# Kernel tuning notes

Hardware: AMD Instinct MI355X
Metric: run time of the kernel (lower is better)

## Reference

```python
import jax, jax.numpy as jnp
import numpy as np

K = 11          # kernel_size
SIGMA = 1.5
CH = 3          # image channels


def _gaussian_kernel(ch):
    coords = jnp.arange(K, dtype=jnp.float32) - (K - 1) / 2
    g = jnp.exp(-coords ** 2 / (2 * SIGMA ** 2))
    g = g / g.sum()
    k2d = jnp.outer(g, g)                       # [K, K]
    return jnp.tile(k2d[None, None], (ch, 1, 1, 1))  # [C, 1, K, K] depthwise


def setup_inputs() -> dict:
    key = jax.random.key(0)
    kx, ky = jax.random.split(key)
    x = jax.random.normal(kx, (32, CH, 512, 512), dtype=jnp.float32)
    y = jax.random.normal(ky, (32, CH, 512, 512), dtype=jnp.float32)
    kernel = _gaussian_kernel(CH)
    return {"x": x, "y": y, "kernel": kernel}


def _blur(v, kernel):
    # depthwise 2D Gaussian blur, SAME padding (K odd)
    c = v.shape[1]
    pad = K // 2
    return jax.lax.conv_general_dilated(
        v, kernel, window_strides=(1, 1), padding=[(pad, pad), (pad, pad)],
        dimension_numbers=("NCHW", "OIHW", "NCHW"), feature_group_count=c)


def reference(x, y, kernel):
    C1 = 0.01 ** 2
    C2 = 0.03 ** 2
    mu_x = _blur(x, kernel)
    mu_y = _blur(y, kernel)
    sigma_x = _blur(x * x, kernel) - mu_x ** 2
    sigma_y = _blur(y * y, kernel) - mu_y ** 2
    sigma_xy = _blur(x * y, kernel) - mu_x * mu_y
    ssim_num = (2 * mu_x * mu_y + C1) * (2 * sigma_xy + C2)
    ssim_den = (mu_x ** 2 + mu_y ** 2 + C1) * (sigma_x + sigma_y + C2)
    ssim = ssim_num / (ssim_den + 1e-8)
    return ((1.0 - ssim) / 2.0).mean()
```

## Files before the change

kernel.cpp:

```cpp
#include <hip/hip_runtime.h>
#include <hip/hip_bf16.h>

#define IMG    512
#define KSZ    11
#define HALO   5
#define STRIP  64
#define PANEL  16
#define NSTEP  (IMG/PANEL)
#define RRING  48
#define RPAIR  24
#define FCOLS  74
#define FSTR   88

typedef short bf16x8 __attribute__((ext_vector_type(8)));
typedef float f32x4  __attribute__((ext_vector_type(4)));

union S8 { bf16x8 v; ushort u16[8]; uint u32[4]; };

__device__ __forceinline__ ushort f2bf(float f) {
    union { __hip_bfloat16 h; ushort u; } c;
    c.h = __float2bfloat16(f);
    return c.u;
}


__global__ __launch_bounds__(256)
void dssim_mfma_kernel(const float* __restrict__ x,
                       const float* __restrict__ y,
                       const float* __restrict__ kern,
                       float* __restrict__ out)
{
    __shared__ float  sgf[16];
    __shared__ ushort gext[64];
    __shared__ ushort Fbuf[5][PANEL][FSTR];
    __shared__ ushort Ring[RPAIR][5][68][2];
    __shared__ float  wsum[4];

    const int tid = threadIdx.x;
    const int l   = tid & 63;
    const int wv  = tid >> 6;
    const int q   = l >> 4;
    const int cj  = l & 15;
    const int wcb = wv * 16 + cj;

    if (tid < KSZ) {
        float s = 0.f;
        #pragma unroll
        for (int j = 0; j < KSZ; ++j) s += kern[tid * KSZ + j];
        sgf[tid] = s;
    }
    for (int i = tid; i < 5 * PANEL * FSTR / 2; i += 256) ((uint*)Fbuf)[i] = 0u;
    for (int i = tid; i < 3 * 5 * 68; i += 256) ((uint*)Ring)[i] = 0u;
    __syncthreads();

    if (tid < 64) {
        const int d = tid - 16;
        gext[tid] = (d >= 0 && d < KSZ) ? f2bf(sgf[d]) : (ushort)0;
    }
    __syncthreads();

    S8 tg;
    #pragma unroll
    for (int ii = 0; ii < 8; ++ii)
        tg.u16[ii] = gext[16 + q * 8 + ii - cj];

    const int plane  = blockIdx.z;
    const int cstrip = blockIdx.x * STRIP;
    const int base   = plane * (IMG * IMG);

    const int srow = tid >> 4;
    const int scol = tid & 15;
    int  gcols[5]; bool coks[5];
    #pragma unroll
    for (int m = 0; m < 5; ++m) {
        const int cl = scol + 16 * m;
        gcols[m] = cstrip - HALO + cl;
        coks[m]  = (cl < FCOLS) && (gcols[m] >= 0) && (gcols[m] < IMG);
    }
    float2 pf[5];

    const ushort* aptr = &Fbuf[0][cj][wv * 16 + q * 8];

    const float C1 = 1e-4f, C2 = 9e-4f;
    const f32x4 z = {0.f, 0.f, 0.f, 0.f};
    float local = 0.f;

    {
        const int r  = srow;
        const int rb = base + r * IMG;
        #pragma unroll
        for (int m = 0; m < 5; ++m) {
            float xv = 0.f, yv = 0.f;
            if (coks[m]) { xv = x[rb + gcols[m]]; yv = y[rb + gcols[m]]; }
            pf[m] = make_float2(xv, yv);
        }
        #pragma unroll
        for (int m = 0; m < 5; ++m) {
            const int cl = scol + 16 * m;
            if (cl < FCOLS) {
                const float fx = pf[m].x, fy = pf[m].y;
                Fbuf[0][srow][cl] = f2bf(fx);
                Fbuf[1][srow][cl] = f2bf(fy);
                Fbuf[2][srow][cl] = f2bf(fx * fx);
                Fbuf[3][srow][cl] = f2bf(fy * fy);
                Fbuf[4][srow][cl] = f2bf(fx * fy);
            }
        }
    }
    __syncthreads();

    for (int t = 0; t <= NSTEP; ++t) {
        {
            const int pb = 16 * (t % 3) + HALO;
            #pragma unroll
            for (int f = 0; f < 5; ++f) {
                S8 a;
                a.v = *(const bf16x8*)(aptr + f * (PANEL * FSTR));
                f32x4 d = __builtin_amdgcn_mfma_f32_16x16x32_bf16(a.v, tg.v, z, 0, 0, 0);
                #pragma unroll
                for (int r = 0; r < 4; ++r) {
                    int rr = pb + q * 4 + r;
                    if (rr >= RRING) rr -= RRING;
                    Ring[rr >> 1][f][wcb][rr & 1] = f2bf(d[r]);
                }
            }
        }

        if (t < NSTEP) {
            const int r   = (t + 1) * PANEL + srow;
            const bool rok = (r < IMG);
            const int rb  = base + r * IMG;
            #pragma unroll
            for (int m = 0; m < 5; ++m) {
                float xv = 0.f, yv = 0.f;
                if (rok && coks[m]) { xv = x[rb + gcols[m]]; yv = y[rb + gcols[m]]; }
                pf[m] = make_float2(xv, yv);
            }
        }

        __syncthreads();

        if (t >= 1) {
            const int s   = t - 1;
            const int pbs = (8 * s) % RPAIR;
            int pr[4];
            #pragma unroll
            for (int ii = 0; ii < 4; ++ii) {
                int v = pbs + q * 4 + ii;
                if (v >= RPAIR) v -= RPAIR;
                pr[ii] = v;
            }
            f32x4 vf[5];
            #pragma unroll
            for (int f = 0; f < 5; ++f) {
                S8 b;
                #pragma unroll
                for (int ii = 0; ii < 4; ++ii)
                    b.u32[ii] = *(const uint*)&Ring[pr[ii]][f][wcb][0];
                vf[f] = __builtin_amdgcn_mfma_f32_16x16x32_bf16(tg.v, b.v, z, 0, 0, 0);
            }
            #pragma unroll
            for (int r = 0; r < 4; ++r) {
                const float mx  = vf[0][r], my  = vf[1][r];
                const float exx = vf[2][r], eyy = vf[3][r], exy = vf[4][r];
                const float sxv = fmaf(-mx, mx, exx);
                const float syv = fmaf(-my, my, eyy);
                const float sxy = fmaf(-mx, my, exy);
                const float num = fmaf(2.f, mx * my, C1) * fmaf(2.f, sxy, C2);
                const float den = fmaf(mx, mx, fmaf(my, my, C1)) * (sxv + syv + C2);
                const float ssim = __fdividef(num, den + 1e-8f);
                local += (1.f - ssim) * 0.5f;
            }
        }

        if (t < NSTEP) {
            #pragma unroll
            for (int m = 0; m < 5; ++m) {
                const int cl = scol + 16 * m;
                if (cl < FCOLS) {
                    const float fx = pf[m].x, fy = pf[m].y;
                    Fbuf[0][srow][cl] = f2bf(fx);
                    Fbuf[1][srow][cl] = f2bf(fy);
                    Fbuf[2][srow][cl] = f2bf(fx * fx);
                    Fbuf[3][srow][cl] = f2bf(fy * fy);
                    Fbuf[4][srow][cl] = f2bf(fx * fy);
                }
            }
        }
        __syncthreads();
    }

    #pragma unroll
    for (int o = 32; o > 0; o >>= 1) local += __shfl_down(local, o, 64);
    if (l == 0) wsum[wv] = local;
    __syncthreads();
    if (tid == 0) {
        const float s = wsum[0] + wsum[1] + wsum[2] + wsum[3];
        atomicAdd(out, s * (1.f / 25165824.f));
    }
}

extern "C" void kernel_launch(void* const* d_in, const int* in_sizes, int n_in,
                              void* d_out, int out_size, void* d_ws, size_t ws_size,
                              hipStream_t stream)
{
    const float* x    = (const float*)d_in[0];
    const float* y    = (const float*)d_in[1];
    const float* kern = (const float*)d_in[2];
    float* out = (float*)d_out;

    hipMemsetAsync(out, 0, sizeof(float), stream);

    dim3 grid(IMG / STRIP, 1, 32 * 3);
    dssim_mfma_kernel<<<grid, 256, 0, stream>>>(x, y, kern, out);
}
```

Measured before the change: 92.42 us.

## Pack bf16 pairs into 32-bit LDS words for staging and ring buffers

Restructures the shared-memory staging so each thread loads column pairs and writes packed bf16x2 words using v_cvt_pk_bf16_f32 and v_pk_mul_f32, instead of scalar 16-bit stores. The ring buffer becomes a flat 32-bit array, with the horizontal MFMA output stored as two packed words and the vertical tap vector shifted by one to match the new row alignment. The aim is fewer LDS store instructions and conversion ops per panel. It risks index or alignment mistakes in the remapped ring offsets and new bank-conflict patterns.

```diff
diff --git a/kernel.cpp b/kernel.cpp
--- a/kernel.cpp
+++ b/kernel.cpp
@@ -6,17 +6,26 @@
 #define HALO   5
 #define STRIP  64
 #define PANEL  16
-#define NSTEP  (IMG/PANEL)
-#define RRING  48
-#define RPAIR  24
-#define FCOLS  74
-#define FSTR   88
+#define NSTEP  32
+#define PAIRS  37
+#define FSTR32 44
+#define FROW   704
+#define RSTR32 340
 
 typedef short bf16x8 __attribute__((ext_vector_type(8)));
 typedef float f32x4  __attribute__((ext_vector_type(4)));
-
 union S8 { bf16x8 v; ushort u16[8]; uint u32[4]; };
 
+__device__ __forceinline__ uint cvtpk(float lo, float hi) {
+    uint r;
+    asm("v_cvt_pk_bf16_f32 %0, %1, %2" : "=v"(r) : "v"(lo), "v"(hi));
+    return r;
+}
+__device__ __forceinline__ float2 pk_mul(float2 a, float2 b) {
+    float2 d;
+    asm("v_pk_mul_f32 %0, %1, %2" : "=v"(d) : "v"(a), "v"(b));
+    return d;
+}
 __device__ __forceinline__ ushort f2bf(float f) {
     union { __hip_bfloat16 h; ushort u; } c;
     c.h = __float2bfloat16(f);
@@ -32,8 +41,8 @@
 {
     __shared__ float  sgf[16];
     __shared__ ushort gext[64];
-    __shared__ ushort Fbuf[5][PANEL][FSTR];
-    __shared__ ushort Ring[RPAIR][5][68][2];
+    __shared__ uint   Fbuf32[5 * FROW];
+    __shared__ uint   Ring32[24 * RSTR32];
     __shared__ float  wsum[4];
 
     const int tid = threadIdx.x;
@@ -49,115 +58,116 @@
         for (int j = 0; j < KSZ; ++j) s += kern[tid * KSZ + j];
         sgf[tid] = s;
     }
-    for (int i = tid; i < 5 * PANEL * FSTR / 2; i += 256) ((uint*)Fbuf)[i] = 0u;
-    for (int i = tid; i < 3 * 5 * 68; i += 256) ((uint*)Ring)[i] = 0u;
-    __syncthreads();
-
+    for (int i = tid; i < 5 * FROW; i += 256) Fbuf32[i] = 0u;
+    for (int i = tid; i < 3 * RSTR32; i += 256) Ring32[i] = 0u;
+    __syncthreads();
     if (tid < 64) {
         const int d = tid - 16;
         gext[tid] = (d >= 0 && d < KSZ) ? f2bf(sgf[d]) : (ushort)0;
     }
     __syncthreads();
 
-    S8 tg;
+    S8 tgh, tgv;
     #pragma unroll
-    for (int ii = 0; ii < 8; ++ii)
-        tg.u16[ii] = gext[16 + q * 8 + ii - cj];
+    for (int ii = 0; ii < 8; ++ii) {
+        tgh.u16[ii] = gext[16 + q * 8 + ii - cj];
+        tgv.u16[ii] = gext[15 + q * 8 + ii - cj];
+    }
 
     const int plane  = blockIdx.z;
     const int cstrip = blockIdx.x * STRIP;
     const int base   = plane * (IMG * IMG);
 
     const int srow = tid >> 4;
-    const int scol = tid & 15;
-    int  gcols[5]; bool coks[5];
+    const int sp   = tid & 15;
+    int gcol0[3], gcol1[3], wo[3];
+    bool ok0[3], ok1[3];
     #pragma unroll
-    for (int m = 0; m < 5; ++m) {
-        const int cl = scol + 16 * m;
-        gcols[m] = cstrip - HALO + cl;
-        coks[m]  = (cl < FCOLS) && (gcols[m] >= 0) && (gcols[m] < IMG);
-    }
-    float2 pf[5];
-
-    const ushort* aptr = &Fbuf[0][cj][wv * 16 + q * 8];
-
+    for (int m = 0; m < 3; ++m) {
+        const int p  = sp + 16 * m;
+        const bool pa = (p < PAIRS);
+        const int c0 = cstrip - HALO + 2 * p;
+        gcol0[m] = c0;  gcol1[m] = c0 + 1;
+        ok0[m] = pa && (c0 >= 0) && (c0 < IMG);
+        ok1[m] = pa && (c0 + 1 >= 0) && (c0 + 1 < IMG);
+        wo[m]  = srow * FSTR32 + p;
+    }
+    float2 px[3], py[3];
+
+    auto prefetch = [&](int pn) {
+        const int r    = pn * PANEL + srow;
+        const bool rok = (r < IMG);
+        const int rb   = base + r * IMG;
+        #pragma unroll
+        for (int m = 0; m < 3; ++m) {
+            float a0 = 0.f, a1 = 0.f, b0 = 0.f, b1 = 0.f;
+            if (rok && ok0[m]) { a0 = x[rb + gcol0[m]]; b0 = y[rb + gcol0[m]]; }
+            if (rok && ok1[m]) { a1 = x[rb + gcol1[m]]; b1 = y[rb + gcol1[m]]; }
+            px[m] = make_float2(a0, a1);
+            py[m] = make_float2(b0, b1);
+        }
+    };
+    auto commit = [&]() {
+        #pragma unroll
+        for (int m = 0; m < 3; ++m) {
+            if (m < 2 || sp < PAIRS - 32) {
+                const float2 vx = px[m], vy = py[m];
+                const float2 xx = pk_mul(vx, vx);
+                const float2 yy = pk_mul(vy, vy);
+                const float2 xy = pk_mul(vx, vy);
+                Fbuf32[0 * FROW + wo[m]] = cvtpk(vx.x, vx.y);
+                Fbuf32[1 * FROW + wo[m]] = cvtpk(vy.x, vy.y);
+                Fbuf32[2 * FROW + wo[m]] = cvtpk(xx.x, xx.y);
+                Fbuf32[3 * FROW + wo[m]] = cvtpk(yy.x, yy.y);
+                Fbuf32[4 * FROW + wo[m]] = cvtpk(xy.x, xy.y);
+            }
+        }
+    };
+
+    prefetch(0);
+    commit();
+    __syncthreads();
+
+    const f32x4 z0 = {0.f, 0.f, 0.f, 0.f};
     const float C1 = 1e-4f, C2 = 9e-4f;
-    const f32x4 z = {0.f, 0.f, 0.f, 0.f};
+    const int aoff = cj * FSTR32 + wv * 8 + q * 4;
     float local = 0.f;
-
-    {
-        const int r  = srow;
-        const int rb = base + r * IMG;
-        #pragma unroll
-        for (int m = 0; m < 5; ++m) {
-            float xv = 0.f, yv = 0.f;
-            if (coks[m]) { xv = x[rb + gcols[m]]; yv = y[rb + gcols[m]]; }
-            pf[m] = make_float2(xv, yv);
-        }
-        #pragma unroll
-        for (int m = 0; m < 5; ++m) {
-            const int cl = scol + 16 * m;
-            if (cl < FCOLS) {
-                const float fx = pf[m].x, fy = pf[m].y;
-                Fbuf[0][srow][cl] = f2bf(fx);
-                Fbuf[1][srow][cl] = f2bf(fy);
-                Fbuf[2][srow][cl] = f2bf(fx * fx);
-                Fbuf[3][srow][cl] = f2bf(fy * fy);
-                Fbuf[4][srow][cl] = f2bf(fx * fy);
-            }
-        }
-    }
-    __syncthreads();
+    int hb = 0, vb = 16;
 
     for (int t = 0; t <= NSTEP; ++t) {
         {
-            const int pb = 16 * (t % 3) + HALO;
+            int p0 = hb + 2 * q + 3;  if (p0 >= 24) p0 -= 24;
+            int p1 = p0 + 1;          if (p1 >= 24) p1 -= 24;
+            const int rw0 = p0 * RSTR32 + wcb;
+            const int rw1 = p1 * RSTR32 + wcb;
             #pragma unroll
             for (int f = 0; f < 5; ++f) {
                 S8 a;
-                a.v = *(const bf16x8*)(aptr + f * (PANEL * FSTR));
-                f32x4 d = __builtin_amdgcn_mfma_f32_16x16x32_bf16(a.v, tg.v, z, 0, 0, 0);
-                #pragma unroll
-                for (int r = 0; r < 4; ++r) {
-                    int rr = pb + q * 4 + r;
-                    if (rr >= RRING) rr -= RRING;
-                    Ring[rr >> 1][f][wcb][rr & 1] = f2bf(d[r]);
-                }
-            }
-        }
-
-        if (t < NSTEP) {
-            const int r   = (t + 1) * PANEL + srow;
-            const bool rok = (r < IMG);
-            const int rb  = base + r * IMG;
-            #pragma unroll
-            for (int m = 0; m < 5; ++m) {
-                float xv = 0.f, yv = 0.f;
-                if (rok && coks[m]) { xv = x[rb + gcols[m]]; yv = y[rb + gcols[m]]; }
-                pf[m] = make_float2(xv, yv);
-            }
-        }
+                a.v = *(const bf16x8*)&Fbuf32[f * FROW + aoff];
+                f32x4 d = __builtin_amdgcn_mfma_f32_16x16x32_bf16(a.v, tgh.v, z0, 0, 0, 0);
+                Ring32[rw0 + f * 68] = cvtpk(d[0], d[1]);
+                Ring32[rw1 + f * 68] = cvtpk(d[2], d[3]);
+            }
+        }
+
+        if (t < NSTEP) prefetch(t + 1);
 
         __syncthreads();
 
         if (t >= 1) {
-            const int s   = t - 1;
-            const int pbs = (8 * s) % RPAIR;
-            int pr[4];
+            int vr[4];
             #pragma unroll
             for (int ii = 0; ii < 4; ++ii) {
-                int v = pbs + q * 4 + ii;
-                if (v >= RPAIR) v -= RPAIR;
-                pr[ii] = v;
+                int pp = vb + 4 * q + ii;  if (pp >= 24) pp -= 24;
+                vr[ii] = pp * RSTR32 + wcb;
             }
             f32x4 vf[5];
             #pragma unroll
             for (int f = 0; f < 5; ++f) {
                 S8 b;
                 #pragma unroll
-                for (int ii = 0; ii < 4; ++ii)
-                    b.u32[ii] = *(const uint*)&Ring[pr[ii]][f][wcb][0];
-                vf[f] = __builtin_amdgcn_mfma_f32_16x16x32_bf16(tg.v, b.v, z, 0, 0, 0);
+                for (int ii = 0; ii < 4; ++ii) b.u32[ii] = Ring32[vr[ii] + f * 68];
+                vf[f] = __builtin_amdgcn_mfma_f32_16x16x32_bf16(tgv.v, b.v, z0, 0, 0, 0);
             }
             #pragma unroll
             for (int r = 0; r < 4; ++r) {
@@ -173,21 +183,11 @@
             }
         }
 
-        if (t < NSTEP) {
-            #pragma unroll
-            for (int m = 0; m < 5; ++m) {
-                const int cl = scol + 16 * m;
-                if (cl < FCOLS) {
-                    const float fx = pf[m].x, fy = pf[m].y;
-                    Fbuf[0][srow][cl] = f2bf(fx);
-                    Fbuf[1][srow][cl] = f2bf(fy);
-                    Fbuf[2][srow][cl] = f2bf(fx * fx);
-                    Fbuf[3][srow][cl] = f2bf(fy * fy);
-                    Fbuf[4][srow][cl] = f2bf(fx * fy);
-                }
-            }
-        }
+        if (t < NSTEP) commit();
         __syncthreads();
+
+        vb = hb;
+        hb += 8;  if (hb >= 24) hb -= 24;
     }
 
     #pragma unroll
```

After: 81.54 us. 11.8% less time.
